# Kernel optimization log

Hardware: AMD Instinct MI355X
Metric: run time of the kernel (lower is better)

Reference implementation:

```python
import jax, jax.numpy as jnp
import numpy as np
import jax.lax as lax

KERNEL = 7
STRIDE = 1
PAD = 3

def setup_inputs() -> dict:
    key = jax.random.key(0)
    kx, kw = jax.random.split(key)
    x = jax.random.normal(kx, (64, 512, 512), dtype=jnp.float32)
    weight = jax.random.normal(kw, (KERNEL, KERNEL), dtype=jnp.float32)
    return {"x": x, "weight": weight}

def reference(x, weight):
    # x: [B, H, W] single-channel; weight: [k, k]
    # Original computes cross-correlation (no kernel flip) with zero padding.
    lhs = x[:, None, :, :]                      # [B, 1, H, W]
    rhs = weight[None, None, :, :]              # [O=1, I=1, k, k]
    out = lax.conv_general_dilated(
        lhs, rhs,
        window_strides=(STRIDE, STRIDE),
        padding=[(PAD, PAD), (PAD, PAD)],
        dimension_numbers=("NCHW", "OIHW", "NCHW"),
    )
    return out[:, 0, :, :]                      # [B, H_out, W_out]
```

## Files before the change

kernel.cpp:

```cpp
#include <hip/hip_runtime.h>


#define IMG_W 512
#define IMG_H 512
#define NIMG  64
#define TW    256
#define TH    32
#define HALO  3
#define LDS_W 264
#define LDS_H (TH + 2*HALO)
#define NF4   (LDS_W / 4)

__global__ __launch_bounds__(256, 4) void conv7x7_kernel(
    const float* __restrict__ x,
    const float* __restrict__ wgt,
    float* __restrict__ out)
{
    __shared__ float tile[LDS_H * LDS_W];

    const int tid = threadIdx.x;
    const int bx  = blockIdx.x * TW;
    const int by  = blockIdx.y * TH;
    const int n   = blockIdx.z;

    const float* img = x + (size_t)n * (IMG_W * IMG_H);

    for (int i = tid; i < LDS_H * NF4; i += 256) {
        const int r  = i / NF4;
        const int c4 = i - r * NF4;
        const int gy = by - HALO + r;
        const int gx = bx - 4 + c4 * 4;
        float4 v = make_float4(0.f, 0.f, 0.f, 0.f);
        if ((unsigned)gy < IMG_H && (unsigned)gx < IMG_W)
            v = *(const float4*)&img[gy * IMG_W + gx];
        *(float4*)&tile[r * LDS_W + c4 * 4] = v;
    }

    float w[49];
    #pragma unroll
    for (int i = 0; i < 49; ++i) w[i] = wgt[i];

    __syncthreads();

    const int tx = tid & 63;
    const int ty = tid >> 6;
    const int lx = tx * 4;
    const int rbase = ty * 8;

    float acc[8][4] = {};

    #pragma unroll
    for (int r = 0; r < 14; ++r) {
        const float* rp = &tile[(rbase + r) * LDS_W + lx];
        const float4 a  = *(const float4*)(rp);
        const float4 b  = *(const float4*)(rp + 4);
        const float4 c4 = *(const float4*)(rp + 8);
        const float row[12] = { a.x, a.y, a.z, a.w,
                                b.x, b.y, b.z, b.w,
                                c4.x, c4.y, c4.z, c4.w };
        #pragma unroll
        for (int j = 0; j < 8; ++j) {
            const int ky = r - j;
            if (ky >= 0 && ky < 7) {
                #pragma unroll
                for (int kx = 0; kx < 7; ++kx) {
                    const float wv = w[ky * 7 + kx];
                    #pragma unroll
                    for (int c = 0; c < 4; ++c)
                        acc[j][c] = fmaf(row[c + kx + 1], wv, acc[j][c]);
                }
            }
        }
    }

    float* o = out + (size_t)n * (IMG_W * IMG_H);
    #pragma unroll
    for (int j = 0; j < 8; ++j) {
        float4 v = make_float4(acc[j][0], acc[j][1], acc[j][2], acc[j][3]);
        *(float4*)&o[(by + rbase + j) * IMG_W + bx + lx] = v;
    }
}

extern "C" void kernel_launch(void* const* d_in, const int* in_sizes, int n_in,
                              void* d_out, int out_size, void* d_ws, size_t ws_size,
                              hipStream_t stream)
{
    const float* x   = (const float*)d_in[0];
    const float* wgt = (const float*)d_in[1];
    float* out       = (float*)d_out;

    dim3 grid(IMG_W / TW, IMG_H / TH, NIMG);
    conv7x7_kernel<<<grid, 256, 0, stream>>>(x, wgt, out);
}
```

Baseline: 133.9 us.

## Drop LDS tiling and load conv rows directly from global memory

Removes the shared-memory tile and barrier; each thread now reads its 14 input rows (three float4 each, with boundary masking) straight from global memory and relies on the L1/L2 caches for halo reuse. Blocks now cover full image width with two 8-row strips, which changes the grid mapping. This removes the LDS staging and sync cost, but global loads are redundant (each row is fetched by several threads and blocks), so it depends on cache hit rates.

Result: slower. 283.0 us (+111.3%).

```diff
diff --git a/kernel.cpp b/kernel.cpp
--- a/kernel.cpp
+++ b/kernel.cpp
@@ -4,62 +4,45 @@
 #define IMG_W 512
 #define IMG_H 512
 #define NIMG  64
-#define TW    256
-#define TH    32
+#define ROWS  8
 #define HALO  3
-#define LDS_W 264
-#define LDS_H (TH + 2*HALO)
-#define NF4   (LDS_W / 4)
 
 __global__ __launch_bounds__(256, 4) void conv7x7_kernel(
     const float* __restrict__ x,
     const float* __restrict__ wgt,
     float* __restrict__ out)
 {
-    __shared__ float tile[LDS_H * LDS_W];
-
     const int tid = threadIdx.x;
-    const int bx  = blockIdx.x * TW;
-    const int by  = blockIdx.y * TH;
-    const int n   = blockIdx.z;
+    const int ox = (tid & 127) * 4;
+    const int ty = tid >> 7;
+    const int oy = (blockIdx.x * 2 + ty) * ROWS;
+    const int n  = blockIdx.y;
 
     const float* img = x + (size_t)n * (IMG_W * IMG_H);
-
-    for (int i = tid; i < LDS_H * NF4; i += 256) {
-        const int r  = i / NF4;
-        const int c4 = i - r * NF4;
-        const int gy = by - HALO + r;
-        const int gx = bx - 4 + c4 * 4;
-        float4 v = make_float4(0.f, 0.f, 0.f, 0.f);
-        if ((unsigned)gy < IMG_H && (unsigned)gx < IMG_W)
-            v = *(const float4*)&img[gy * IMG_W + gx];
-        *(float4*)&tile[r * LDS_W + c4 * 4] = v;
-    }
 
     float w[49];
     #pragma unroll
     for (int i = 0; i < 49; ++i) w[i] = wgt[i];
 
-    __syncthreads();
+    const bool lval = (ox != 0);
+    const bool rval = (ox + 7 < IMG_W);
 
-    const int tx = tid & 63;
-    const int ty = tid >> 6;
-    const int lx = tx * 4;
-    const int rbase = ty * 8;
-
-    float acc[8][4] = {};
+    float acc[ROWS][4] = {};
+    const float4 z4 = make_float4(0.f, 0.f, 0.f, 0.f);
 
     #pragma unroll
-    for (int r = 0; r < 14; ++r) {
-        const float* rp = &tile[(rbase + r) * LDS_W + lx];
-        const float4 a  = *(const float4*)(rp);
-        const float4 b  = *(const float4*)(rp + 4);
-        const float4 c4 = *(const float4*)(rp + 8);
+    for (int r = 0; r < ROWS + 2 * HALO; ++r) {
+        const int gy = oy - HALO + r;
+        const bool yv = (unsigned)gy < IMG_H;
+        const float* rp = &img[(size_t)gy * IMG_W + ox];
+        const float4 a  = (yv && lval) ? *(const float4*)(rp - 4) : z4;
+        const float4 b  = yv           ? *(const float4*)(rp)     : z4;
+        const float4 c4 = (yv && rval) ? *(const float4*)(rp + 4) : z4;
         const float row[12] = { a.x, a.y, a.z, a.w,
                                 b.x, b.y, b.z, b.w,
                                 c4.x, c4.y, c4.z, c4.w };
         #pragma unroll
-        for (int j = 0; j < 8; ++j) {
+        for (int j = 0; j < ROWS; ++j) {
             const int ky = r - j;
             if (ky >= 0 && ky < 7) {
                 #pragma unroll
@@ -75,9 +58,9 @@
 
     float* o = out + (size_t)n * (IMG_W * IMG_H);
     #pragma unroll
-    for (int j = 0; j < 8; ++j) {
+    for (int j = 0; j < ROWS; ++j) {
         float4 v = make_float4(acc[j][0], acc[j][1], acc[j][2], acc[j][3]);
-        *(float4*)&o[(by + rbase + j) * IMG_W + bx + lx] = v;
+        *(float4*)&o[(size_t)(oy + j) * IMG_W + ox] = v;
     }
 }
 
@@ -89,6 +72,6 @@
     const float* wgt = (const float*)d_in[1];
     float* out       = (float*)d_out;
 
-    dim3 grid(IMG_W / TW, IMG_H / TH, NIMG);
+    dim3 grid(IMG_H / (2 * ROWS), NIMG, 1);
     conv7x7_kernel<<<grid, 256, 0, stream>>>(x, wgt, out);
 }
```
